# Kernel tuning notes

Measured on AMD Instinct MI355X. Metric: run time of the kernel, lower is better.

## Reference

```python
import jax, jax.numpy as jnp
import numpy as np

VX, VY = 0.16, 0.16
PC_RANGE = (0.0, -39.68, -3.0, 69.12, 39.68, 1.0)
X_OFFSET = VX / 2.0 + PC_RANGE[0]
Y_OFFSET = VY / 2.0 + PC_RANGE[1]
BN_EPS = 1e-3


def setup_inputs() -> dict:
    key = jax.random.key(0)
    k1, k2, k3, k4, k5, k6 = jax.random.split(key, 6)
    P, N, C_IN, C_AUG, C_OUT = 30000, 32, 4, 9, 64
    inputs = jax.random.normal(k1, (P, N, C_IN), dtype=jnp.float32)
    num_points = jnp.maximum(jax.random.randint(k2, (P,), 0, N, dtype=jnp.int32), 1)
    coords = jax.random.randint(k3, (P, 4), 0, 432, dtype=jnp.int32)
    # PFN layer params: Linear(9->64, no bias), BatchNorm1d(64) affine params
    W = jax.random.normal(k4, (C_AUG, C_OUT), dtype=jnp.float32) * (1.0 / np.sqrt(C_AUG))
    gamma = jnp.ones((C_OUT,), dtype=jnp.float32) + 0.1 * jax.random.normal(k5, (C_OUT,), dtype=jnp.float32)
    beta = 0.1 * jax.random.normal(k6, (C_OUT,), dtype=jnp.float32)
    return {"inputs": inputs, "num_points": num_points, "coords": coords,
            "W": W, "gamma": gamma, "beta": beta}


def reference(inputs, num_points, coords, W, gamma, beta):
    # inputs: (P, N, 4); num_points: (P,); coords: (P, 4) = (batch, z, y, x)
    P, N, _ = inputs.shape
    dtype = inputs.dtype
    npf = num_points.astype(dtype)

    # cluster offsets: per-pillar mean of xyz (sum over all N slots / num_points, as in source)
    points_mean = inputs[:, :, :3].sum(axis=1, keepdims=True) / npf[:, None, None]
    f_cluster = inputs[:, :, :3] - points_mean  # (P, N, 3)

    # center offsets w.r.t. pillar center
    cx = coords[:, 3].astype(dtype)[:, None] * VX + X_OFFSET  # (P, 1)
    cy = coords[:, 2].astype(dtype)[:, None] * VY + Y_OFFSET
    f_center = jnp.stack([inputs[:, :, 0] - cx, inputs[:, :, 1] - cy], axis=-1)  # (P, N, 2)

    feats = jnp.concatenate([inputs, f_cluster, f_center], axis=-1)  # (P, N, 9)

    # zero out padding points
    mask = (jnp.arange(N)[None, :] < num_points[:, None]).astype(dtype)[:, :, None]
    feats = feats * mask

    # PFNLayer: linear -> BatchNorm1d (training-mode batch stats over P*N) -> ReLU -> max over points
    x = jnp.einsum('pnc,cd->pnd', feats, W)  # (P, N, 64)
    mean = x.mean(axis=(0, 1))
    var = jnp.mean(jnp.square(x - mean), axis=(0, 1))  # biased, as torch BN
    x = (x - mean) * jax.lax.rsqrt(var + BN_EPS) * gamma + beta
    x = jax.nn.relu(x)
    return x.max(axis=1)  # (P, 64)
```

## Files before the change

### kernel.cpp

```cpp
#include <hip/hip_runtime.h>
#include <math.h>


#define NSLOT 32
#define NCH 64
#define NREP 8
#define META_OFF 512

static constexpr float kVX = 0.16f, kVY = 0.16f;
static constexpr float kXOff = 0.08f;
static constexpr float kYOff = 0.08f - 39.68f;
static constexpr float kEps = 1e-3f;
static constexpr float kNegInf = -3.402823466e38f;

__global__ __launch_bounds__(256) void k_stats(const float* __restrict__ in,
                                               const int* __restrict__ npts,
                                               const int* __restrict__ coords,
                                               float* __restrict__ ws,
                                               float* __restrict__ meta, int P) {
    const int tid = threadIdx.x;
    const int lane = tid & 63;
    const int wv = tid >> 6;
    const int sub = lane & 3;
    const int pi = blockIdx.x * 64 + wv * 16 + (lane >> 2);
    const bool valid = pi < P;

    float T0 = 0.f, T1 = 0.f, T2 = 0.f;
    float S0 = 0.f, S1 = 0.f, S2 = 0.f, S3 = 0.f;
    float Q[10];
#pragma unroll
    for (int i = 0; i < 10; ++i) Q[i] = 0.f;
    int np = 1;
    float cx = 0.f, cy = 0.f, npf = 1.f;

    if (valid) {
        np = npts[pi];
        np = np < 1 ? 1 : (np > NSLOT ? NSLOT : np);
        npf = (float)np;
        const int4 cd = *reinterpret_cast<const int4*>(coords + (size_t)pi * 4);
        cx = (float)cd.w * kVX + kXOff;
        cy = (float)cd.z * kVY + kYOff;
        const float* bp = in + (size_t)pi * 128 + sub * 4;
#pragma unroll
        for (int k = 0; k < 8; ++k) {
            const float4 u = *reinterpret_cast<const float4*>(bp + k * 16);
            const int slot = sub + k * 4;
            T0 += u.x; T1 += u.y; T2 += u.z;
            const bool m = slot < np;
            const float ax = m ? u.x : 0.f, ay = m ? u.y : 0.f;
            const float az = m ? u.z : 0.f, aw = m ? u.w : 0.f;
            S0 += ax; S1 += ay; S2 += az; S3 += aw;
            Q[0] += ax * u.x; Q[1] += ax * u.y; Q[2] += ax * u.z; Q[3] += ax * u.w;
            Q[4] += ay * u.y; Q[5] += ay * u.z; Q[6] += ay * u.w;
            Q[7] += az * u.z; Q[8] += az * u.w;
            Q[9] += aw * u.w;
        }
    }

#define QUADR(v) { v += __shfl_xor(v, 1); v += __shfl_xor(v, 2); }
    QUADR(T0) QUADR(T1) QUADR(T2)
    QUADR(S0) QUADR(S1) QUADR(S2) QUADR(S3)
#pragma unroll
    for (int i = 0; i < 10; ++i) QUADR(Q[i])
#undef QUADR

    float acc[54];
#pragma unroll
    for (int i = 0; i < 54; ++i) acc[i] = 0.f;

    if (valid && sub == 0) {
        const float mx = T0 / npf, my = T1 / npf, mz = T2 / npf;
        if (meta) {
            *reinterpret_cast<float4*>(meta + (size_t)pi * 8) =
                make_float4(mx, my, mz, npf);
            *reinterpret_cast<float4*>(meta + (size_t)pi * 8 + 4) =
                make_float4(cx, cy, 0.f, 0.f);
        }
        const float AS[9] = {S0, S1, S2, S3, S0, S1, S2, S0, S1};
        const float b9[9] = {0.f, 0.f, 0.f, 0.f, -mx, -my, -mz, -cx, -cy};
        const int r9[9] = {0, 1, 2, 3, 0, 1, 2, 0, 1};
        float Qm[4][4];
        Qm[0][0] = Q[0]; Qm[0][1] = Q[1]; Qm[0][2] = Q[2]; Qm[0][3] = Q[3];
        Qm[1][0] = Q[1]; Qm[1][1] = Q[4]; Qm[1][2] = Q[5]; Qm[1][3] = Q[6];
        Qm[2][0] = Q[2]; Qm[2][1] = Q[5]; Qm[2][2] = Q[7]; Qm[2][3] = Q[8];
        Qm[3][0] = Q[3]; Qm[3][1] = Q[6]; Qm[3][2] = Q[8]; Qm[3][3] = Q[9];
#pragma unroll
        for (int i = 0; i < 9; ++i) acc[i] = AS[i] + npf * b9[i];
        int k = 9;
#pragma unroll
        for (int i = 0; i < 9; ++i)
#pragma unroll
            for (int j = i; j < 9; ++j) {
                acc[k] = Qm[r9[i]][r9[j]] + AS[i] * b9[j] + b9[i] * AS[j]
                         + npf * b9[i] * b9[j];
                ++k;
            }
    }

#pragma unroll
    for (int i = 0; i < 54; ++i) {
        acc[i] += __shfl_xor(acc[i], 4);
        acc[i] += __shfl_xor(acc[i], 8);
        acc[i] += __shfl_xor(acc[i], 16);
        acc[i] += __shfl_xor(acc[i], 32);
    }

    __shared__ float red[4][54];
    if (lane == 0) {
#pragma unroll
        for (int i = 0; i < 54; ++i) red[wv][i] = acc[i];
    }
    __syncthreads();
    if (tid < 54) {
        const float v = red[0][tid] + red[1][tid] + red[2][tid] + red[3][tid];
        atomicAdd(&ws[(blockIdx.x & (NREP - 1)) * 64 + tid], v);
    }
}

__device__ __forceinline__ float dot4(const float4 u, float V0, float V1,
                                      float V2, float V3, float c0) {
    return fmaf(u.x, V0, fmaf(u.y, V1, fmaf(u.z, V2, fmaf(u.w, V3, c0))));
}

template <bool MEANS>
__global__ __launch_bounds__(256) void k_out(const float* __restrict__ in,
                                             const int* __restrict__ npts,
                                             const int* __restrict__ coords,
                                             const float* __restrict__ W,
                                             const float* __restrict__ gamma,
                                             const float* __restrict__ beta,
                                             const float* __restrict__ ws,
                                             const float* __restrict__ meta,
                                             float* __restrict__ out, int P) {
    __shared__ float ssum[54];
    __shared__ float lds[4][128];
    const int tid = threadIdx.x;
    const int lane = tid & 63;
    const int wv = tid >> 6;
    const int gwave = blockIdx.x * 4 + wv;
    const int nwave = gridDim.x * 4;
    const int d = lane;

    if (tid < 54) {
        float v = 0.f;
#pragma unroll
        for (int r = 0; r < NREP; ++r) v += ws[r * 64 + tid];
        ssum[tid] = v;
    }
    __syncthreads();

    float Wc[9];
#pragma unroll
    for (int c = 0; c < 9; ++c) Wc[c] = W[c * NCH + d];

    const float invPN = 1.0f / ((float)P * (float)NSLOT);
    float mean = 0.f;
#pragma unroll
    for (int c = 0; c < 9; ++c) mean += ssum[c] * Wc[c];
    mean *= invPN;

    float e2 = 0.f;
    {
        int k = 9;
#pragma unroll
        for (int i = 0; i < 9; ++i)
#pragma unroll
            for (int j = i; j < 9; ++j) {
                const float coef = (i == j) ? 1.f : 2.f;
                e2 += coef * ssum[k] * Wc[i] * Wc[j];
                ++k;
            }
    }
    e2 *= invPN;
    const float var = e2 - mean * mean;
    const float s = gamma[d] * rsqrtf(var + kEps);
    const float t = beta[d] - mean * s;

    const float V0 = s * (Wc[0] + Wc[4] + Wc[7]);
    const float V1 = s * (Wc[1] + Wc[5] + Wc[8]);
    const float V2 = s * (Wc[2] + Wc[6]);
    const float V3 = s * Wc[3];
    const float sW4 = s * Wc[4], sW5 = s * Wc[5], sW6 = s * Wc[6];
    const float sW7 = s * Wc[7], sW8 = s * Wc[8];

    if (MEANS) {
        int p = gwave;
        float2 g = make_float2(0.f, 0.f);
        float4 m1 = make_float4(0.f, 0.f, 0.f, 1.f);
        float4 m2 = make_float4(0.f, 0.f, 0.f, 0.f);
        if (p < P) {
            g = *reinterpret_cast<const float2*>(in + (size_t)p * 128 + lane * 2);
            m1 = *reinterpret_cast<const float4*>(meta + (size_t)p * 8);
            m2 = *reinterpret_cast<const float4*>(meta + (size_t)p * 8 + 4);
        }
        while (p < P) {
            *reinterpret_cast<float2*>(&lds[wv][lane * 2]) = g;
            const int pn = p + nwave;
            float2 gn = make_float2(0.f, 0.f);
            float4 m1n = make_float4(0.f, 0.f, 0.f, 1.f);
            float4 m2n = make_float4(0.f, 0.f, 0.f, 0.f);
            if (pn < P) {
                gn = *reinterpret_cast<const float2*>(in + (size_t)pn * 128 + lane * 2);
                m1n = *reinterpret_cast<const float4*>(meta + (size_t)pn * 8);
                m2n = *reinterpret_cast<const float4*>(meta + (size_t)pn * 8 + 4);
            }
            const int np = (int)m1.w;
            const float c0 = t - (m1.x * sW4 + m1.y * sW5 + m1.z * sW6 +
                                  m2.x * sW7 + m2.y * sW8);
            const float* L = lds[wv];
            float y0 = (np < NSLOT) ? t : kNegInf;
            float y1 = kNegInf, y2 = kNegInf, y3 = kNegInf;
            int n = 0;
            for (; n + 4 <= np; n += 4) {
                const float4 u0 = *reinterpret_cast<const float4*>(L + n * 4);
                const float4 u1 = *reinterpret_cast<const float4*>(L + n * 4 + 4);
                const float4 u2 = *reinterpret_cast<const float4*>(L + n * 4 + 8);
                const float4 u3 = *reinterpret_cast<const float4*>(L + n * 4 + 12);
                y0 = fmaxf(y0, dot4(u0, V0, V1, V2, V3, c0));
                y1 = fmaxf(y1, dot4(u1, V0, V1, V2, V3, c0));
                y2 = fmaxf(y2, dot4(u2, V0, V1, V2, V3, c0));
                y3 = fmaxf(y3, dot4(u3, V0, V1, V2, V3, c0));
            }
            for (; n < np; ++n) {
                const float4 u0 = *reinterpret_cast<const float4*>(L + n * 4);
                y0 = fmaxf(y0, dot4(u0, V0, V1, V2, V3, c0));
            }
            out[(size_t)p * NCH + d] =
                fmaxf(fmaxf(fmaxf(y0, y1), fmaxf(y2, y3)), 0.f);
            p = pn; g = gn; m1 = m1n; m2 = m2n;
        }
    } else {
        for (int p = gwave; p < P; p += nwave) {
            const float2 g = *reinterpret_cast<const float2*>(in + (size_t)p * 128 + lane * 2);
            int np = npts[p];
            np = np < 1 ? 1 : (np > NSLOT ? NSLOT : np);
            const bool ev = !(lane & 1);
            float px = ev ? g.x : 0.f;
            float py = ev ? g.y : 0.f;
            float pz = ev ? 0.f : g.x;
#pragma unroll
            for (int m = 1; m < 64; m <<= 1) {
                px += __shfl_xor(px, m);
                py += __shfl_xor(py, m);
                pz += __shfl_xor(pz, m);
            }
            const float npf = (float)np;
            const float mx = px / npf, my = py / npf, mz = pz / npf;
            const int4 cd = *reinterpret_cast<const int4*>(coords + (size_t)p * 4);
            const float cx = (float)cd.w * kVX + kXOff;
            const float cy = (float)cd.z * kVY + kYOff;
            const float c0 = t - (mx * sW4 + my * sW5 + mz * sW6 + cx * sW7 + cy * sW8);
            *reinterpret_cast<float2*>(&lds[wv][lane * 2]) = g;
            const float* L = lds[wv];
            float y0 = (np < NSLOT) ? t : kNegInf;
            float y1 = kNegInf;
            int n = 0;
            for (; n + 2 <= np; n += 2) {
                const float4 u0 = *reinterpret_cast<const float4*>(L + n * 4);
                const float4 u1 = *reinterpret_cast<const float4*>(L + n * 4 + 4);
                y0 = fmaxf(y0, dot4(u0, V0, V1, V2, V3, c0));
                y1 = fmaxf(y1, dot4(u1, V0, V1, V2, V3, c0));
            }
            if (n < np) {
                const float4 u0 = *reinterpret_cast<const float4*>(L + n * 4);
                y0 = fmaxf(y0, dot4(u0, V0, V1, V2, V3, c0));
            }
            out[(size_t)p * NCH + d] = fmaxf(fmaxf(y0, y1), 0.f);
        }
    }
}

extern "C" void kernel_launch(void* const* d_in, const int* in_sizes, int n_in,
                              void* d_out, int out_size, void* d_ws, size_t ws_size,
                              hipStream_t stream) {
    const float* in = (const float*)d_in[0];
    const int* npts = (const int*)d_in[1];
    const int* coords = (const int*)d_in[2];
    const float* W = (const float*)d_in[3];
    const float* gamma = (const float*)d_in[4];
    const float* beta = (const float*)d_in[5];
    float* out = (float*)d_out;
    float* ws = (float*)d_ws;
    const int P = in_sizes[1];

    const size_t need = (META_OFF + 8 * (size_t)P) * sizeof(float);
    const bool means = ws_size >= need;
    float* meta = means ? (ws + META_OFF) : nullptr;

    hipMemsetAsync(ws, 0, META_OFF * sizeof(float), stream);
    const int sblocks = (P + 63) / 64;
    k_stats<<<sblocks, 256, 0, stream>>>(in, npts, coords, ws, meta, P);
    if (means) {
        k_out<true><<<2048, 256, 0, stream>>>(in, npts, coords, W, gamma, beta, ws,
                                              meta, out, P);
    } else {
        k_out<false><<<2048, 256, 0, stream>>>(in, npts, coords, W, gamma, beta, ws,
                                               meta, out, P);
    }
}
```

Baseline: 31.94 us.

## Read pillar points via wave-uniform scalar loads instead of LDS staging

```diff
diff --git a/kernel.cpp b/kernel.cpp
--- a/kernel.cpp
+++ b/kernel.cpp
@@ -30,11 +30,10 @@
     float Q[10];
 #pragma unroll
     for (int i = 0; i < 10; ++i) Q[i] = 0.f;
-    int np = 1;
     float cx = 0.f, cy = 0.f, npf = 1.f;
 
     if (valid) {
-        np = npts[pi];
+        int np = npts[pi];
         np = np < 1 ? 1 : (np > NSLOT ? NSLOT : np);
         npf = (float)np;
         const int4 cd = *reinterpret_cast<const int4*>(coords + (size_t)pi * 4);
@@ -69,7 +68,8 @@
     for (int i = 0; i < 54; ++i) acc[i] = 0.f;
 
     if (valid && sub == 0) {
-        const float mx = T0 / npf, my = T1 / npf, mz = T2 / npf;
+        const float inv = 1.0f / npf;
+        const float mx = T0 * inv, my = T1 * inv, mz = T2 * inv;
         if (meta) {
             *reinterpret_cast<float4*>(meta + (size_t)pi * 8) =
                 make_float4(mx, my, mz, npf);
@@ -133,7 +133,6 @@
                                              const float* __restrict__ meta,
                                              float* __restrict__ out, int P) {
     __shared__ float ssum[54];
-    __shared__ float lds[4][128];
     const int tid = threadIdx.x;
     const int lane = tid & 63;
     const int wv = tid >> 6;
@@ -183,90 +182,53 @@
     const float sW4 = s * Wc[4], sW5 = s * Wc[5], sW6 = s * Wc[6];
     const float sW7 = s * Wc[7], sW8 = s * Wc[8];
 
-    if (MEANS) {
-        int p = gwave;
-        float2 g = make_float2(0.f, 0.f);
-        float4 m1 = make_float4(0.f, 0.f, 0.f, 1.f);
-        float4 m2 = make_float4(0.f, 0.f, 0.f, 0.f);
-        if (p < P) {
-            g = *reinterpret_cast<const float2*>(in + (size_t)p * 128 + lane * 2);
-            m1 = *reinterpret_cast<const float4*>(meta + (size_t)p * 8);
-            m2 = *reinterpret_cast<const float4*>(meta + (size_t)p * 8 + 4);
-        }
-        while (p < P) {
-            *reinterpret_cast<float2*>(&lds[wv][lane * 2]) = g;
-            const int pn = p + nwave;
-            float2 gn = make_float2(0.f, 0.f);
-            float4 m1n = make_float4(0.f, 0.f, 0.f, 1.f);
-            float4 m2n = make_float4(0.f, 0.f, 0.f, 0.f);
-            if (pn < P) {
-                gn = *reinterpret_cast<const float2*>(in + (size_t)pn * 128 + lane * 2);
-                m1n = *reinterpret_cast<const float4*>(meta + (size_t)pn * 8);
-                m2n = *reinterpret_cast<const float4*>(meta + (size_t)pn * 8 + 4);
+    const float4* __restrict__ in4 = reinterpret_cast<const float4*>(in);
+
+    for (int p = gwave; p < P; p += nwave) {
+        const int pu = __builtin_amdgcn_readfirstlane(p);
+        float mx, my, mz, cx, cy;
+        int np;
+        if (MEANS) {
+            const float4 m1 = *reinterpret_cast<const float4*>(meta + (size_t)pu * 8);
+            const float4 m2 = *reinterpret_cast<const float4*>(meta + (size_t)pu * 8 + 4);
+            mx = m1.x; my = m1.y; mz = m1.z; np = (int)m1.w;
+            cx = m2.x; cy = m2.y;
+        } else {
+            np = npts[pu];
+            np = np < 1 ? 1 : (np > NSLOT ? NSLOT : np);
+            float T0 = 0.f, T1 = 0.f, T2 = 0.f;
+            for (int n = 0; n < NSLOT; ++n) {
+                const float4 u = in4[(size_t)pu * 32 + n];
+                T0 += u.x; T1 += u.y; T2 += u.z;
             }
-            const int np = (int)m1.w;
-            const float c0 = t - (m1.x * sW4 + m1.y * sW5 + m1.z * sW6 +
-                                  m2.x * sW7 + m2.y * sW8);
-            const float* L = lds[wv];
-            float y0 = (np < NSLOT) ? t : kNegInf;
-            float y1 = kNegInf, y2 = kNegInf, y3 = kNegInf;
-            int n = 0;
-            for (; n + 4 <= np; n += 4) {
-                const float4 u0 = *reinterpret_cast<const float4*>(L + n * 4);
-                const float4 u1 = *reinterpret_cast<const float4*>(L + n * 4 + 4);
-                const float4 u2 = *reinterpret_cast<const float4*>(L + n * 4 + 8);
-                const float4 u3 = *reinterpret_cast<const float4*>(L + n * 4 + 12);
-                y0 = fmaxf(y0, dot4(u0, V0, V1, V2, V3, c0));
-                y1 = fmaxf(y1, dot4(u1, V0, V1, V2, V3, c0));
-                y2 = fmaxf(y2, dot4(u2, V0, V1, V2, V3, c0));
-                y3 = fmaxf(y3, dot4(u3, V0, V1, V2, V3, c0));
-            }
-            for (; n < np; ++n) {
-                const float4 u0 = *reinterpret_cast<const float4*>(L + n * 4);
-                y0 = fmaxf(y0, dot4(u0, V0, V1, V2, V3, c0));
-            }
-            out[(size_t)p * NCH + d] =
-                fmaxf(fmaxf(fmaxf(y0, y1), fmaxf(y2, y3)), 0.f);
-            p = pn; g = gn; m1 = m1n; m2 = m2n;
-        }
-    } else {
-        for (int p = gwave; p < P; p += nwave) {
-            const float2 g = *reinterpret_cast<const float2*>(in + (size_t)p * 128 + lane * 2);
-            int np = npts[p];
-            np = np < 1 ? 1 : (np > NSLOT ? NSLOT : np);
-            const bool ev = !(lane & 1);
-            float px = ev ? g.x : 0.f;
-            float py = ev ? g.y : 0.f;
-            float pz = ev ? 0.f : g.x;
-#pragma unroll
-            for (int m = 1; m < 64; m <<= 1) {
-                px += __shfl_xor(px, m);
-                py += __shfl_xor(py, m);
-                pz += __shfl_xor(pz, m);
-            }
-            const float npf = (float)np;
-            const float mx = px / npf, my = py / npf, mz = pz / npf;
-            const int4 cd = *reinterpret_cast<const int4*>(coords + (size_t)p * 4);
-            const float cx = (float)cd.w * kVX + kXOff;
-            const float cy = (float)cd.z * kVY + kYOff;
-            const float c0 = t - (mx * sW4 + my * sW5 + mz * sW6 + cx * sW7 + cy * sW8);
-            *reinterpret_cast<float2*>(&lds[wv][lane * 2]) = g;
-            const float* L = lds[wv];
-            float y0 = (np < NSLOT) ? t : kNegInf;
-            float y1 = kNegInf;
-            int n = 0;
-            for (; n + 2 <= np; n += 2) {
-                const float4 u0 = *reinterpret_cast<const float4*>(L + n * 4);
-                const float4 u1 = *reinterpret_cast<const float4*>(L + n * 4 + 4);
-                y0 = fmaxf(y0, dot4(u0, V0, V1, V2, V3, c0));
-                y1 = fmaxf(y1, dot4(u1, V0, V1, V2, V3, c0));
-            }
-            if (n < np) {
-                const float4 u0 = *reinterpret_cast<const float4*>(L + n * 4);
-                y0 = fmaxf(y0, dot4(u0, V0, V1, V2, V3, c0));
-            }
-            out[(size_t)p * NCH + d] = fmaxf(fmaxf(y0, y1), 0.f);
-        }
+            const float inv = 1.0f / (float)np;
+            mx = T0 * inv; my = T1 * inv; mz = T2 * inv;
+            const int4 cd = *reinterpret_cast<const int4*>(coords + (size_t)pu * 4);
+            cx = (float)cd.w * kVX + kXOff;
+            cy = (float)cd.z * kVY + kYOff;
+        }
+        const float c0 = t - (mx * sW4 + my * sW5 + mz * sW6 + cx * sW7 + cy * sW8);
+        const float4* __restrict__ U = in4 + (size_t)pu * 32;
+
+        float y0 = (np < NSLOT) ? t : kNegInf;
+        float y1 = kNegInf, y2 = kNegInf, y3 = kNegInf;
+        int n = 0;
+        for (; n + 4 <= np; n += 4) {
+            const float4 u0 = U[n];
+            const float4 u1 = U[n + 1];
+            const float4 u2 = U[n + 2];
+            const float4 u3 = U[n + 3];
+            y0 = fmaxf(y0, dot4(u0, V0, V1, V2, V3, c0));
+            y1 = fmaxf(y1, dot4(u1, V0, V1, V2, V3, c0));
+            y2 = fmaxf(y2, dot4(u2, V0, V1, V2, V3, c0));
+            y3 = fmaxf(y3, dot4(u3, V0, V1, V2, V3, c0));
+        }
+        for (; n < np; ++n) {
+            const float4 u0 = U[n];
+            y0 = fmaxf(y0, dot4(u0, V0, V1, V2, V3, c0));
+        }
+        out[(size_t)pu * NCH + d] =
+            fmaxf(fmaxf(fmaxf(y0, y1), fmaxf(y2, y3)), 0.f);
     }
 }
 
@@ -291,10 +253,10 @@
     const int sblocks = (P + 63) / 64;
     k_stats<<<sblocks, 256, 0, stream>>>(in, npts, coords, ws, meta, P);
     if (means) {
-        k_out<true><<<2048, 256, 0, stream>>>(in, npts, coords, W, gamma, beta, ws,
+        k_out<true><<<1024, 256, 0, stream>>>(in, npts, coords, W, gamma, beta, ws,
                                               meta, out, P);
     } else {
-        k_out<false><<<2048, 256, 0, stream>>>(in, npts, coords, W, gamma, beta, ws,
+        k_out<false><<<1024, 256, 0, stream>>>(in, npts, coords, W, gamma, beta, ws,
                                                meta, out, P);
     }
 }
```

After: 38.19 us. 19.6% more time.

## Replace atomic stat reduction with per-block partials and single-block fold kernel

Applied to the files above, without the earlier changes.

```diff
diff --git a/kernel.cpp b/kernel.cpp
--- a/kernel.cpp
+++ b/kernel.cpp
@@ -4,8 +4,6 @@
 
 #define NSLOT 32
 #define NCH 64
-#define NREP 8
-#define META_OFF 512
 
 static constexpr float kVX = 0.16f, kVY = 0.16f;
 static constexpr float kXOff = 0.08f;
@@ -16,7 +14,7 @@
 __global__ __launch_bounds__(256) void k_stats(const float* __restrict__ in,
                                                const int* __restrict__ npts,
                                                const int* __restrict__ coords,
-                                               float* __restrict__ ws,
+                                               float* __restrict__ part,
                                                float* __restrict__ meta, int P) {
     const int tid = threadIdx.x;
     const int lane = tid & 63;
@@ -30,11 +28,10 @@
     float Q[10];
 #pragma unroll
     for (int i = 0; i < 10; ++i) Q[i] = 0.f;
-    int np = 1;
     float cx = 0.f, cy = 0.f, npf = 1.f;
 
     if (valid) {
-        np = npts[pi];
+        int np = npts[pi];
         np = np < 1 ? 1 : (np > NSLOT ? NSLOT : np);
         npf = (float)np;
         const int4 cd = *reinterpret_cast<const int4*>(coords + (size_t)pi * 4);
@@ -69,7 +66,8 @@
     for (int i = 0; i < 54; ++i) acc[i] = 0.f;
 
     if (valid && sub == 0) {
-        const float mx = T0 / npf, my = T1 / npf, mz = T2 / npf;
+        const float inv = 1.0f / npf;
+        const float mx = T0 * inv, my = T1 * inv, mz = T2 * inv;
         if (meta) {
             *reinterpret_cast<float4*>(meta + (size_t)pi * 8) =
                 make_float4(mx, my, mz, npf);
@@ -112,8 +110,66 @@
     }
     __syncthreads();
     if (tid < 54) {
-        const float v = red[0][tid] + red[1][tid] + red[2][tid] + red[3][tid];
-        atomicAdd(&ws[(blockIdx.x & (NREP - 1)) * 64 + tid], v);
+        part[(size_t)blockIdx.x * 64 + tid] =
+            red[0][tid] + red[1][tid] + red[2][tid] + red[3][tid];
+    }
+}
+
+__global__ __launch_bounds__(256) void k_mid(const float* __restrict__ part,
+                                             const float* __restrict__ W,
+                                             const float* __restrict__ gamma,
+                                             const float* __restrict__ beta,
+                                             float* __restrict__ fold,
+                                             int nb, int P) {
+    __shared__ float sred[4][64];
+    __shared__ float ssum[64];
+    const int tid = threadIdx.x;
+    const int e = tid & 63;
+    const int grp = tid >> 6;
+    float v = 0.f;
+    if (e < 54) {
+        for (int i = grp; i < nb; i += 4) v += part[(size_t)i * 64 + e];
+    }
+    sred[grp][e] = v;
+    __syncthreads();
+    if (tid < 64)
+        ssum[tid] = sred[0][tid] + sred[1][tid] + sred[2][tid] + sred[3][tid];
+    __syncthreads();
+
+    if (tid < 64) {
+        const int d = tid;
+        float Wc[9];
+#pragma unroll
+        for (int c = 0; c < 9; ++c) Wc[c] = W[c * NCH + d];
+        const float invPN = 1.0f / ((float)P * (float)NSLOT);
+        float mean = 0.f;
+#pragma unroll
+        for (int c = 0; c < 9; ++c) mean += ssum[c] * Wc[c];
+        mean *= invPN;
+        float e2 = 0.f;
+        int k = 9;
+#pragma unroll
+        for (int i = 0; i < 9; ++i)
+#pragma unroll
+            for (int j = i; j < 9; ++j) {
+                const float coef = (i == j) ? 1.f : 2.f;
+                e2 += coef * ssum[k] * Wc[i] * Wc[j];
+                ++k;
+            }
+        e2 *= invPN;
+        const float var = e2 - mean * mean;
+        const float s = gamma[d] * rsqrtf(var + kEps);
+        const float t = beta[d] - mean * s;
+        fold[0 * 64 + d] = s * (Wc[0] + Wc[4] + Wc[7]);
+        fold[1 * 64 + d] = s * (Wc[1] + Wc[5] + Wc[8]);
+        fold[2 * 64 + d] = s * (Wc[2] + Wc[6]);
+        fold[3 * 64 + d] = s * Wc[3];
+        fold[4 * 64 + d] = s * Wc[4];
+        fold[5 * 64 + d] = s * Wc[5];
+        fold[6 * 64 + d] = s * Wc[6];
+        fold[7 * 64 + d] = s * Wc[7];
+        fold[8 * 64 + d] = s * Wc[8];
+        fold[9 * 64 + d] = t;
     }
 }
 
@@ -126,62 +182,22 @@
 __global__ __launch_bounds__(256) void k_out(const float* __restrict__ in,
                                              const int* __restrict__ npts,
                                              const int* __restrict__ coords,
-                                             const float* __restrict__ W,
-                                             const float* __restrict__ gamma,
-                                             const float* __restrict__ beta,
-                                             const float* __restrict__ ws,
+                                             const float* __restrict__ fold,
                                              const float* __restrict__ meta,
                                              float* __restrict__ out, int P) {
-    __shared__ float ssum[54];
     __shared__ float lds[4][128];
     const int tid = threadIdx.x;
     const int lane = tid & 63;
     const int wv = tid >> 6;
     const int gwave = blockIdx.x * 4 + wv;
     const int nwave = gridDim.x * 4;
-    const int d = lane;
-
-    if (tid < 54) {
-        float v = 0.f;
-#pragma unroll
-        for (int r = 0; r < NREP; ++r) v += ws[r * 64 + tid];
-        ssum[tid] = v;
-    }
-    __syncthreads();
-
-    float Wc[9];
-#pragma unroll
-    for (int c = 0; c < 9; ++c) Wc[c] = W[c * NCH + d];
-
-    const float invPN = 1.0f / ((float)P * (float)NSLOT);
-    float mean = 0.f;
-#pragma unroll
-    for (int c = 0; c < 9; ++c) mean += ssum[c] * Wc[c];
-    mean *= invPN;
-
-    float e2 = 0.f;
-    {
-        int k = 9;
-#pragma unroll
-        for (int i = 0; i < 9; ++i)
-#pragma unroll
-            for (int j = i; j < 9; ++j) {
-                const float coef = (i == j) ? 1.f : 2.f;
-                e2 += coef * ssum[k] * Wc[i] * Wc[j];
-                ++k;
-            }
-    }
-    e2 *= invPN;
-    const float var = e2 - mean * mean;
-    const float s = gamma[d] * rsqrtf(var + kEps);
-    const float t = beta[d] - mean * s;
-
-    const float V0 = s * (Wc[0] + Wc[4] + Wc[7]);
-    const float V1 = s * (Wc[1] + Wc[5] + Wc[8]);
-    const float V2 = s * (Wc[2] + Wc[6]);
-    const float V3 = s * Wc[3];
-    const float sW4 = s * Wc[4], sW5 = s * Wc[5], sW6 = s * Wc[6];
-    const float sW7 = s * Wc[7], sW8 = s * Wc[8];
+
+    float F[10];
+#pragma unroll
+    for (int j = 0; j < 10; ++j) F[j] = fold[j * 64 + lane];
+    const float V0 = F[0], V1 = F[1], V2 = F[2], V3 = F[3];
+    const float sW4 = F[4], sW5 = F[5], sW6 = F[6], sW7 = F[7], sW8 = F[8];
+    const float t = F[9];
 
     if (MEANS) {
         int p = gwave;
@@ -225,7 +241,7 @@
                 const float4 u0 = *reinterpret_cast<const float4*>(L + n * 4);
                 y0 = fmaxf(y0, dot4(u0, V0, V1, V2, V3, c0));
             }
-            out[(size_t)p * NCH + d] =
+            out[(size_t)p * NCH + lane] =
                 fmaxf(fmaxf(fmaxf(y0, y1), fmaxf(y2, y3)), 0.f);
             p = pn; g = gn; m1 = m1n; m2 = m2n;
         }
@@ -265,7 +281,7 @@
                 const float4 u0 = *reinterpret_cast<const float4*>(L + n * 4);
                 y0 = fmaxf(y0, dot4(u0, V0, V1, V2, V3, c0));
             }
-            out[(size_t)p * NCH + d] = fmaxf(fmaxf(y0, y1), 0.f);
+            out[(size_t)p * NCH + lane] = fmaxf(fmaxf(y0, y1), 0.f);
         }
     }
 }
@@ -283,18 +299,19 @@
     float* ws = (float*)d_ws;
     const int P = in_sizes[1];
 
-    const size_t need = (META_OFF + 8 * (size_t)P) * sizeof(float);
-    const bool means = ws_size >= need;
-    float* meta = means ? (ws + META_OFF) : nullptr;
-
-    hipMemsetAsync(ws, 0, META_OFF * sizeof(float), stream);
-    const int sblocks = (P + 63) / 64;
-    k_stats<<<sblocks, 256, 0, stream>>>(in, npts, coords, ws, meta, P);
+    const int nb = (P + 63) / 64;
+    const size_t foff = (size_t)nb * 64;
+    const size_t moff = (foff + 640 + 63) & ~(size_t)63;
+    float* part = ws;
+    float* fold = ws + foff;
+    const bool means = ws_size >= (moff + 8 * (size_t)P) * sizeof(float);
+    float* meta = means ? (ws + moff) : nullptr;
+
+    k_stats<<<nb, 256, 0, stream>>>(in, npts, coords, part, meta, P);
+    k_mid<<<1, 256, 0, stream>>>(part, W, gamma, beta, fold, nb, P);
     if (means) {
-        k_out<true><<<2048, 256, 0, stream>>>(in, npts, coords, W, gamma, beta, ws,
-                                              meta, out, P);
+        k_out<true><<<2048, 256, 0, stream>>>(in, npts, coords, fold, meta, out, P);
     } else {
-        k_out<false><<<2048, 256, 0, stream>>>(in, npts, coords, W, gamma, beta, ws,
-                                               meta, out, P);
-    }
-}
+        k_out<false><<<2048, 256, 0, stream>>>(in, npts, coords, fold, meta, out, P);
+    }
+}
```

Result: slower. 53.57 us (+67.7%).
